# Kernel tuning notes

Measured on AMD Instinct MI355X. Metric: run time of the kernel, lower is better.

The kernel has to match this reference:

```python
import jax, jax.numpy as jnp
import numpy as np

B, N, H, DK, DV = 2, 2048, 16, 128, 128
E = H * DV
EPS = 1e-6


def setup_inputs() -> dict:
    key = jax.random.key(0)
    ks = jax.random.split(key, 8)
    sc_qk = 1.0 / np.sqrt(E + H * DK)  # xavier_normal-ish std
    sc_e = 1.0 / np.sqrt(2 * E)
    d = {
        "x": jax.random.normal(ks[0], (B, N, E), jnp.float32),
        "Wq": jax.random.normal(ks[1], (H * DK, E), jnp.float32) * sc_qk,
        "bq": jnp.zeros((H * DK,), jnp.float32),
        "Wk": jax.random.normal(ks[2], (H * DK, E), jnp.float32) * sc_qk,
        "bk": jnp.zeros((H * DK,), jnp.float32),
        "Wv": jax.random.normal(ks[3], (E, E), jnp.float32) * sc_e,
        "bv": jnp.zeros((E,), jnp.float32),
        "Wg": jax.random.normal(ks[4], (E, E), jnp.float32) * sc_e,
        "bg": jnp.zeros((E,), jnp.float32),
        "Wo": jax.random.normal(ks[5], (E, E), jnp.float32) * sc_e,
        "bo": jnp.zeros((E,), jnp.float32),
        "start_idx": 0,
    }
    return d


def _retention_scan(q, k, v, decays):
    # q,k: [B,N,H,DK] (k already scaled), v: [B,N,H,DV]
    qs = jnp.moveaxis(q, 1, 0)  # [N,B,H,DK]
    ks_ = jnp.moveaxis(k, 1, 0)
    vs = jnp.moveaxis(v, 1, 0)
    dec = decays[None, :, None, None]  # [1,H,1,1]

    def step(state, qkv):
        qt, kt, vt = qkv
        # state_n = decay * state_{n-1} + k_n (x) v_n
        state = dec * state + kt[..., :, None] * vt[..., None, :]  # [B,H,DK,DV]
        ret = jnp.einsum("bhk,bhkv->bhv", qt, state)
        return state, ret

    init = jnp.zeros((q.shape[0], H, DK, DV), q.dtype)
    final_state, rets = jax.lax.scan(step, init, (qs, ks_, vs))
    return jnp.moveaxis(rets, 0, 1), final_state  # [B,N,H,DV], [B,H,DK,DV]


def reference(x, Wq, bq, Wk, bk, Wv, bv, Wg, bg, Wo, bo, start_idx):
    b, n, _ = x.shape
    decays = 1.0 - jnp.exp2(-5.0 - jnp.arange(H, dtype=jnp.float32))  # [H]
    q = (x @ Wq.T + bq).reshape(b, n, H, DK)
    k = (x @ Wk.T + bk).reshape(b, n, H, DK) / (DK ** 0.5)
    v = (x @ Wv.T + bv).reshape(b, n, H, DV)
    retention, state = _retention_scan(q, k, v, decays)
    # GroupNorm over (b n) tokens, num_groups=H, channels=E, no affine
    r = retention.reshape(b * n, H, DV).astype(jnp.float32)
    mu = jnp.mean(r, axis=-1, keepdims=True)
    var = jnp.var(r, axis=-1, keepdims=True)
    r = (r - mu) / jnp.sqrt(var + EPS)
    r = r.reshape(b, n, E).astype(x.dtype)
    gate = jax.nn.silu(x @ Wg.T + bg)
    out = (r * gate) @ Wo.T + bo
    return out, state
```

## Files before the change

kernel.cpp:

```cpp
#include <hip/hip_runtime.h>
#include <hip/hip_bf16.h>

typedef __attribute__((ext_vector_type(8))) short short8;
typedef __attribute__((ext_vector_type(4))) short short4v;
typedef __attribute__((ext_vector_type(4))) float floatx4;

#define DI __device__ __forceinline__

constexpr int B_ = 2, N_ = 2048, H_ = 16, DK_ = 128, DV_ = 128, E_ = 2048;
constexpr int M_ = B_ * N_;
constexpr int NCAT_ = 4 * E_;
constexpr int CH_ = 128;
constexpr int NC_ = N_ / CH_;
constexpr float KSCALE = 0.08838834764831845f;

constexpr long OFF_XB   = 0;
constexpr long OFF_WCAT = 16777216;
constexpr long OFF_WOB  = 50331648;
constexpr long OFF_BCAT = 58720256;
constexpr long OFF_Y    = 58753024;
constexpr long OFF_KT   = 125861888;
constexpr long OFF_VT   = 142639104;
constexpr long OFF_SCB  = 159416320;

DI unsigned short f2bf(float f){
  unsigned u = __float_as_uint(f);
  u += 0x7fffu + ((u >> 16) & 1u);
  return (unsigned short)(u >> 16);
}
DI float bf2f(unsigned short s){ return __uint_as_float(((unsigned)s) << 16); }

DI void gload_lds16(const void* g, void* l){
  __builtin_amdgcn_global_load_lds(
      (const __attribute__((address_space(1))) unsigned int*)g,
      (__attribute__((address_space(3))) unsigned int*)l, 16, 0, 0);
}

__global__ void k_castall(const float* __restrict__ x,
                          const float* __restrict__ Wq, const float* __restrict__ Wk,
                          const float* __restrict__ Wv, const float* __restrict__ Wg,
                          const float* __restrict__ Wo,
                          const float* __restrict__ bq, const float* __restrict__ bk,
                          const float* __restrict__ bv, const float* __restrict__ bg,
                          unsigned short* __restrict__ xb, unsigned short* __restrict__ Wcat,
                          unsigned short* __restrict__ Wob, float* __restrict__ bcat){
  int bid = blockIdx.x;
  if(bid >= 14336){
    int i = (bid - 14336) * 2048 + threadIdx.x * 8;
    #pragma unroll
    for(int u=0;u<8;++u){
      int j = i + u;
      float v;
      if(j < 2048)      v = bq[j];
      else if(j < 4096) v = bk[j - 2048];
      else if(j < 6144) v = bv[j - 4096];
      else              v = bg[j - 6144];
      bcat[j] = v;
    }
    return;
  }
  const float* s; unsigned short* d; long off;
  if(bid < 4096){ s = x; d = xb; off = (long)bid*2048; }
  else if(bid < 6144){ s = Wq; d = Wcat;            off = (long)(bid-4096)*2048; }
  else if(bid < 8192){ s = Wk; d = Wcat + 4194304L; off = (long)(bid-6144)*2048; }
  else if(bid < 10240){ s = Wv; d = Wcat + 8388608L; off = (long)(bid-8192)*2048; }
  else if(bid < 12288){ s = Wg; d = Wcat + 12582912L; off = (long)(bid-10240)*2048; }
  else { s = Wo; d = Wob; off = (long)(bid-12288)*2048; }
  long i = off + (long)threadIdx.x * 8;
  float4 v0 = *(const float4*)(s + i);
  float4 v1 = *(const float4*)(s + i + 4);
  short8 o;
  o[0]=(short)f2bf(v0.x); o[1]=(short)f2bf(v0.y); o[2]=(short)f2bf(v0.z); o[3]=(short)f2bf(v0.w);
  o[4]=(short)f2bf(v1.x); o[5]=(short)f2bf(v1.y); o[6]=(short)f2bf(v1.z); o[7]=(short)f2bf(v1.w);
  *(short8*)(d + i) = o;
}

__global__ __launch_bounds__(512, 2)
void k_gemm256(const unsigned short* __restrict__ A,
               const unsigned short* __restrict__ Bt,
               unsigned short* __restrict__ Y,
               const float* __restrict__ bias)
{
  extern __shared__ unsigned short lds[];
  constexpr int K = 2048;
  constexpr int NKT = K / 64;

  const int tid = threadIdx.x;
  const int wave = tid >> 6, lane = tid & 63;
  const int wr = wave >> 2, wc = wave & 3;
  const int l15 = lane & 15;

  int bid = blockIdx.x;
  int g = bid & 7, w = bid >> 3;
  int bm = (g & 1) * 8 + (w & 7);
  int bn = (g >> 1) * 8 + (w >> 3);

  const unsigned short* Ag = A  + (long)bm * 256 * K;
  const unsigned short* Bg = Bt + (long)bn * 256 * K;

  const int sr = (lane >> 3);
  const int sc = ((lane & 7) ^ sr) * 8;
  const int colx[2] = { ((0 + (lane>>4)) ^ (lane&7)) << 4,
                        ((4 + (lane>>4)) ^ (lane&7)) << 4 };

  floatx4 acc[8][4] = {};
  const char* ldsc = (const char*)lds;
  short8 Aa[8], Ab[8], Ba[4], Bb[4];

#define STG_A(buf, kt, mh) do{                                                        \
    _Pragma("unroll")                                                                 \
    for(int g2=0; g2<2; ++g2){                                                        \
      gload_lds16(Ag + (long)(wr*128 + (mh)*64 + wc*16 + g2*8 + sr)*K                 \
                     + (long)(kt)*64 + sc,                                            \
                  &lds[(buf)*16384 + wr*8192 + ((mh)*64 + wc*16 + g2*8)*64 + lane*8]);\
    }                                                                                 \
  }while(0)

#define STG_B(buf, kt, nh) do{                                                        \
    _Pragma("unroll")                                                                 \
    for(int g2=0; g2<2; ++g2){                                                        \
      gload_lds16(Bg + (long)(wc*64 + (nh)*32 + wr*16 + g2*8 + sr)*K                  \
                     + (long)(kt)*64 + sc,                                            \
                  &lds[32768 + (buf)*16384 + (wc>>1)*8192                             \
                       + ((wc&1)*64 + (nh)*32 + wr*16 + g2*8)*64 + lane*8]);          \
    }                                                                                 \
  }while(0)

#define RD_A(dst, buf, mh) do{                                                        \
    const char* _b = ldsc + ((buf)*16384 + wr*8192)*2;                                \
    _Pragma("unroll")                                                                 \
    for(int ai=0; ai<4; ++ai){                                                        \
      const int _rb = ((mh)*64 + ai*16 + l15) << 7;                                   \
      dst[ai*2+0] = *(const short8*)(_b + _rb + colx[0]);                             \
      dst[ai*2+1] = *(const short8*)(_b + _rb + colx[1]);                             \
    }                                                                                 \
  }while(0)

#define RD_B(dst, buf, nh) do{                                                        \
    const char* _b = ldsc + (32768 + (buf)*16384 + (wc>>1)*8192)*2;                   \
    _Pragma("unroll")                                                                 \
    for(int bj=0; bj<2; ++bj){                                                        \
      const int _rb = ((wc&1)*64 + (nh)*32 + bj*16 + l15) << 7;                       \
      dst[bj*2+0] = *(const short8*)(_b + _rb + colx[0]);                             \
      dst[bj*2+1] = *(const short8*)(_b + _rb + colx[1]);                             \
    }                                                                                 \
  }while(0)

#define MFQ(mh, nh, As, Bs) do{                                                       \
    __builtin_amdgcn_s_setprio(1);                                                    \
    _Pragma("unroll")                                                                 \
    for(int ai=0; ai<4; ++ai)                                                         \
      _Pragma("unroll")                                                               \
      for(int bj=0; bj<2; ++bj)                                                       \
        _Pragma("unroll")                                                             \
        for(int kk=0; kk<2; ++kk)                                                     \
          acc[(mh)*4+ai][(nh)*2+bj] = __builtin_amdgcn_mfma_f32_16x16x32_bf16(        \
              As[ai*2+kk], Bs[bj*2+kk], acc[(mh)*4+ai][(nh)*2+bj], 0,0,0);            \
    __builtin_amdgcn_s_setprio(0);                                                    \
  }while(0)

#define VM4   asm volatile("s_waitcnt vmcnt(4)" ::: "memory")
#define BAR   __builtin_amdgcn_s_barrier()
#define SCHED __builtin_amdgcn_sched_barrier(0)

  STG_A(0, 0, 0); STG_B(0, 0, 0); STG_B(0, 0, 1); STG_A(0, 0, 1);
  VM4;
  BAR;
  SCHED;

  #pragma unroll 1
  for(int i=0; i<NKT/2; ++i){
    const int t1 = 2*i + 1;
    const int t2 = (2*i + 2) & (NKT - 1);

    RD_A(Aa, 0, 0); RD_B(Ba, 0, 0);
    STG_A(1, t1, 0); STG_B(1, t1, 0);
    VM4; BAR;
    MFQ(0, 0, Aa, Ba);
    BAR; SCHED;
    RD_B(Bb, 0, 1);
    STG_B(1, t1, 1);
    VM4; BAR;
    MFQ(0, 1, Aa, Bb);
    BAR; SCHED;
    RD_A(Ab, 0, 1);
    STG_A(1, t1, 1);
    VM4; BAR;
    MFQ(1, 1, Ab, Bb);
    BAR; SCHED;
    VM4; BAR;
    MFQ(1, 0, Ab, Ba);
    BAR; SCHED;

    RD_A(Aa, 1, 0); RD_B(Ba, 1, 0);
    STG_A(0, t2, 0); STG_B(0, t2, 0);
    VM4; BAR;
    MFQ(0, 0, Aa, Ba);
    BAR; SCHED;
    RD_B(Bb, 1, 1);
    STG_B(0, t2, 1);
    VM4; BAR;
    MFQ(0, 1, Aa, Bb);
    BAR; SCHED;
    RD_A(Ab, 1, 1);
    STG_A(0, t2, 1);
    VM4; BAR;
    MFQ(1, 1, Ab, Bb);
    BAR; SCHED;
    VM4; BAR;
    MFQ(1, 0, Ab, Ba);
    BAR; SCHED;
  }
#undef STG_A
#undef STG_B
#undef RD_A
#undef RD_B
#undef MFQ
#undef VM4
#undef BAR
#undef SCHED

  #pragma unroll
  for(int mh=0;mh<2;++mh){
    #pragma unroll
    for(int ai=0;ai<4;++ai){
      const int rowi = bm*256 + wr*128 + mh*64 + ai*16 + ((lane>>4)<<2);
      #pragma unroll
      for(int nh=0;nh<2;++nh){
        #pragma unroll
        for(int bj=0;bj<2;++bj){
          const int col = bn*256 + wc*64 + nh*32 + bj*16 + l15;
          const float bs = bias[col];
          const int sec = col >> 11;
          #pragma unroll
          for(int r=0;r<4;++r){
            float v = acc[mh*4+ai][nh*2+bj][r] + bs;
            if(sec == 1) v *= KSCALE;
            else if(sec == 3) v = v / (1.f + __expf(-v));
            Y[(long)(rowi + r) * NCAT_ + col] = f2bf(v);
          }
        }
      }
    }
  }
}

template<int EPI>
__global__ __launch_bounds__(256)
void k_gemm(const unsigned short* __restrict__ A,
            const unsigned short* __restrict__ Bt,
            void* __restrict__ outp,
            const float* __restrict__ bias,
            int M, int Ncols, int K, int NB)
{
  __shared__ unsigned short lA[2*128*64];
  __shared__ unsigned short lB[2*128*64];
  const int bid = blockIdx.x;
  const int bm = bid / NB, bn = bid % NB;
  const int tid = threadIdx.x;
  const int wave = tid >> 6, lane = tid & 63;
  const int wr = wave >> 1, wc = wave & 1;

  floatx4 acc[4][4] = {};

  int srow[4], scol[4];
  #pragma unroll
  for(int is=0; is<4; ++is){
    int o = is*4096 + wave*1024 + lane*16;
    int row = o >> 7;
    int logcb = (o & 127) ^ ((row & 7) << 4);
    srow[is] = row; scol[is] = logcb >> 1;
  }
  const unsigned short* Abase = A + (long)bm * 128 * K;
  const unsigned short* Bbase = Bt + (long)bn * 128 * K;

#define STG128(kt, buf) do{                                                          \
    const int _k0 = (kt) << 6;                                                       \
    _Pragma("unroll")                                                                \
    for(int is=0; is<4; ++is){                                                       \
      gload_lds16(Abase + (long)srow[is]*K + _k0 + scol[is], &lA[(buf)*8192 + ((is*4096 + wave*1024) >> 1)]); \
      gload_lds16(Bbase + (long)srow[is]*K + _k0 + scol[is], &lB[(buf)*8192 + ((is*4096 + wave*1024) >> 1)]); \
    }                                                                                \
  }while(0)

  const int nkt = K >> 6;
  STG128(0, 0);
  for(int kt=0; kt<nkt; ++kt){
    const int cur = kt & 1, nxt = cur ^ 1;
    const int ktn = (kt + 1 == nkt) ? 0 : kt + 1;
    __syncthreads();
    STG128(ktn, nxt);
    const char* cA = (const char*)lA + cur*16384;
    const char* cB = (const char*)lB + cur*16384;
    #pragma unroll
    for(int kk=0; kk<2; ++kk){
      const int cb = (kk<<6) + ((lane>>4)<<4);
      short8 af[4], bfr[4];
      #pragma unroll
      for(int i=0;i<4;++i){
        int row = (wr<<6) + (i<<4) + (lane&15);
        af[i] = *(const short8*)(cA + (row<<7) + (cb ^ ((row&7)<<4)));
      }
      #pragma unroll
      for(int j=0;j<4;++j){
        int row = (wc<<6) + (j<<4) + (lane&15);
        bfr[j] = *(const short8*)(cB + (row<<7) + (cb ^ ((row&7)<<4)));
      }
      #pragma unroll
      for(int i=0;i<4;++i)
        #pragma unroll
        for(int j=0;j<4;++j)
          acc[i][j] = __builtin_amdgcn_mfma_f32_16x16x32_bf16(af[i], bfr[j], acc[i][j], 0,0,0);
    }
  }
#undef STG128

  #pragma unroll
  for(int i=0;i<4;++i){
    #pragma unroll
    for(int j=0;j<4;++j){
      #pragma unroll
      for(int r=0;r<4;++r){
        int row = bm*128 + (wr<<6) + (i<<4) + ((lane>>4)<<2) + r;
        int col = bn*128 + (wc<<6) + (j<<4) + (lane&15);
        float v = acc[i][j][r] + bias[col];
        if(EPI == 0){
          int sec = col >> 11;
          if(sec == 1) v *= KSCALE;
          else if(sec == 3) v = v / (1.f + __expf(-v));
          ((unsigned short*)outp)[(long)row * Ncols + col] = f2bf(v);
        } else {
          ((float*)outp)[(long)row * Ncols + col] = v;
        }
      }
    }
  }
}

__global__ __launch_bounds__(256)
void k_chunksumT(const unsigned short* __restrict__ Y,
                 unsigned short* __restrict__ Vt,
                 float* __restrict__ MS){
  __shared__ unsigned short lt[64][136];
  __shared__ unsigned short Kt2[128][72];
  __shared__ unsigned short Vt2[128][72];
  int bid = blockIdx.x;
  int bh = bid >> 4, c = bid & 15, b = bh >> 4, h = bh & 15;
  int tid = threadIdx.x, wave = tid >> 6, lane = tid & 63;
  int wr = wave >> 1, wc = wave & 1;
  float dec = 1.f - exp2f(-5.f - (float)h);
  float l2d = log2f(dec);

  floatx4 acc[4][4] = {};

  #pragma unroll 1
  for(int h2 = 0; h2 < 2; ++h2){
    #pragma unroll
    for(int p=0;p<4;++p){
      int tl = p*16 + (tid>>4);
      int t  = h2*64 + tl;
      long row = ((long)(b*N_ + c*CH_ + t))*NCAT_ + 2048 + h*128 + (tid&15)*8;
      short8 v = *(const short8*)(Y + row);
      float f = exp2f(-(float)t * l2d);
      #pragma unroll
      for(int u=0;u<8;++u) v[u] = (short)f2bf(bf2f((unsigned short)v[u]) * f);
      *(short8*)&lt[tl][(tid&15)*8] = v;
    }
    __syncthreads();
    #pragma unroll
    for(int p=0;p<4;++p){
      int dk = p*32 + (tid>>3);
      int tc = (tid&7)*8;
      short8 o;
      #pragma unroll
      for(int u=0;u<8;++u) o[u] = (short)lt[tc+u][dk];
      *(short8*)&Kt2[dk][tc] = o;
    }
    __syncthreads();
    #pragma unroll
    for(int p=0;p<4;++p){
      int tl = p*16 + (tid>>4);
      int t  = h2*64 + tl;
      long row = ((long)(b*N_ + c*CH_ + t))*NCAT_ + 4096 + h*128 + (tid&15)*8;
      *(short8*)&lt[tl][(tid&15)*8] = *(const short8*)(Y + row);
    }
    __syncthreads();
    #pragma unroll
    for(int p=0;p<4;++p){
      int dv = p*32 + (tid>>3);
      int tc = (tid&7)*8;
      short8 o;
      #pragma unroll
      for(int u=0;u<8;++u) o[u] = (short)lt[tc+u][dv];
      *(short8*)&Vt2[dv][tc] = o;
      *(short8*)(Vt + ((long)(bh*128 + dv))*N_ + c*CH_ + h2*64 + tc) = o;
    }
    __syncthreads();
    #pragma unroll
    for(int kk=0;kk<2;++kk){
      int tl = kk*32 + ((lane>>4)<<3);
      short8 af[4], bfr[4];
      #pragma unroll
      for(int i=0;i<4;++i){ int dv = (wr<<6)+(i<<4)+(lane&15); af[i]  = *(const short8*)&Vt2[dv][tl]; }
      #pragma unroll
      for(int j=0;j<4;++j){ int dk = (wc<<6)+(j<<4)+(lane&15); bfr[j] = *(const short8*)&Kt2[dk][tl]; }
      #pragma unroll
      for(int i=0;i<4;++i)
        #pragma unroll
        for(int j=0;j<4;++j)
          acc[i][j] = __builtin_amdgcn_mfma_f32_16x16x32_bf16(af[i], bfr[j], acc[i][j], 0,0,0);
    }
    __syncthreads();
  }

  float scale = exp2f(127.f * log2f(dec));
  float* Mo = MS + ((long)bh*NC_ + c) * 16384;
  #pragma unroll
  for(int i=0;i<4;++i)
    #pragma unroll
    for(int j=0;j<4;++j)
      #pragma unroll
      for(int r=0;r<4;++r){
        int dv = (wr<<6)+(i<<4)+((lane>>4)<<2)+r;
        int dk = (wc<<6)+(j<<4)+(lane&15);
        Mo[dv*128 + dk] = acc[i][j][r] * scale;
      }
}

__global__ __launch_bounds__(256)
void k_scan(const float* __restrict__ MS, unsigned short* __restrict__ Scb,
            float* __restrict__ stateOut){
  int bid = blockIdx.x;
  int bh = bid >> 4, p = bid & 15;
  int tid = threadIdx.x, h = bh & 15;
  float dec = 1.f - exp2f(-5.f - (float)h);
  float decC = exp2f(128.f * log2f(dec));
  int e0 = p*1024 + tid*4;
  floatx4 S = {0.f, 0.f, 0.f, 0.f};
  const float* base = MS + (long)bh * NC_ * 16384 + e0;
  unsigned short* sb = Scb + (long)bh * NC_ * 16384 + e0;
  for(int c=0;c<NC_;++c){
    floatx4 m = *(const floatx4*)(base + (long)c*16384);
    short4v q;
    #pragma unroll
    for(int u=0;u<4;++u) q[u] = (short)f2bf(S[u]);
    *(short4v*)(sb + (long)c*16384) = q;
    S = decC * S + m;
  }
  int dv = e0 >> 7, dk = e0 & 127;
  float* so = stateOut + (long)bh*16384 + dv;
  #pragma unroll
  for(int u=0;u<4;++u) so[(long)(dk+u)*128] = S[u];
}

__global__ __launch_bounds__(256)
void k_ret(const unsigned short* __restrict__ Y, const unsigned short* __restrict__ Vt,
           const unsigned short* __restrict__ Scb, unsigned short* __restrict__ RG){
  __shared__ unsigned short sQ[128*128];
  __shared__ unsigned short sK[128*128];
  int bid = blockIdx.x;
  int bh = bid >> 4, c = bid & 15, b = bh >> 4, h = bh & 15;
  int tid = threadIdx.x, w = tid >> 6, lane = tid & 63;
  float dec = 1.f - exp2f(-5.f - (float)h);
  float l2d = log2f(dec);

  #pragma unroll
  for(int p=0;p<8;++p){
    int t = p*16 + (tid>>4);
    long row = (long)(b*N_ + c*CH_ + t) * NCAT_ + h*128 + (tid&15)*8;
    short8 qv = *(const short8*)(Y + row);
    short8 kv = *(const short8*)(Y + row + 2048);
    float fq = exp2f((float)t * l2d);
    float fk = exp2f(-(float)t * l2d);
    short8 qs, ks;
    #pragma unroll
    for(int u=0;u<8;++u){
      qs[u] = (short)f2bf(bf2f((unsigned short)qv[u]) * fq);
      ks[u] = (short)f2bf(bf2f((unsigned short)kv[u]) * fk);
    }
    int ad = t*256 + (((tid&15)*16) ^ ((t&7)<<4));
    *(short8*)((char*)sQ + ad) = qs;
    *(short8*)((char*)sK + ad) = ks;
  }
  __syncthreads();

  floatx4 acc[2][8] = {};
  #pragma unroll
  for(int kk=0;kk<4;++kk){
    int cb = (kk<<6) + ((lane>>4)<<4);
    short8 af[2], bfr[8];
    #pragma unroll
    for(int i=0;i<2;++i){ int t = w*32 + (i<<4) + (lane&15); af[i] = *(const short8*)((const char*)sQ + t*256 + (cb ^ ((t&7)<<4))); }
    #pragma unroll
    for(int j=0;j<8;++j){ int s = (j<<4) + (lane&15); bfr[j] = *(const short8*)((const char*)sK + s*256 + (cb ^ ((s&7)<<4))); }
    #pragma unroll
    for(int i=0;i<2;++i)
      #pragma unroll
      for(int j=0;j<8;++j)
        acc[i][j] = __builtin_amdgcn_mfma_f32_16x16x32_bf16(af[i], bfr[j], acc[i][j], 0,0,0);
  }
  __syncthreads();

  #pragma unroll
  for(int i=0;i<2;++i)
    #pragma unroll
    for(int j=0;j<8;++j)
      #pragma unroll
      for(int r=0;r<4;++r){
        int t = w*32 + (i<<4) + ((lane>>4)<<2) + r;
        int s = (j<<4) + (lane&15);
        float v = (s <= t) ? acc[i][j][r] : 0.f;
        *(unsigned short*)((char*)sK + t*256 + ((s*2) ^ ((t&7)<<4))) = f2bf(v);
      }
  __syncthreads();

  #pragma unroll
  for(int i=0;i<2;++i)
    #pragma unroll
    for(int j=0;j<8;++j)
      #pragma unroll
      for(int u=0;u<4;++u) acc[i][j][u] = 0.f;

  const unsigned short* Vb = Vt + (long)bh*128*N_ + c*CH_;
  #pragma unroll
  for(int kk=0;kk<4;++kk){
    int cb = (kk<<6) + ((lane>>4)<<4);
    int sg = kk*32 + ((lane>>4)<<3);
    short8 af[2], bfr[8];
    #pragma unroll
    for(int i=0;i<2;++i){ int t = w*32 + (i<<4) + (lane&15); af[i] = *(const short8*)((const char*)sK + t*256 + (cb ^ ((t&7)<<4))); }
    #pragma unroll
    for(int j=0;j<8;++j){ int dv = (j<<4) + (lane&15); bfr[j] = *(const short8*)(Vb + (long)dv*N_ + sg); }
    #pragma unroll
    for(int i=0;i<2;++i)
      #pragma unroll
      for(int j=0;j<8;++j)
        acc[i][j] = __builtin_amdgcn_mfma_f32_16x16x32_bf16(af[i], bfr[j], acc[i][j], 0,0,0);
  }
  const unsigned short* Sb = Scb + ((long)bh*NC_ + c) * 16384;
  #pragma unroll
  for(int kk=0;kk<4;++kk){
    int cb = (kk<<6) + ((lane>>4)<<4);
    int kg = kk*32 + ((lane>>4)<<3);
    short8 af[2], bfr[8];
    #pragma unroll
    for(int i=0;i<2;++i){
      int t = w*32 + (i<<4) + (lane&15);
      short8 qv = *(const short8*)((const char*)sQ + t*256 + (cb ^ ((t&7)<<4)));
      #pragma unroll
      for(int u=0;u<8;++u) af[i][u] = (short)f2bf(bf2f((unsigned short)qv[u]) * dec);
    }
    #pragma unroll
    for(int j=0;j<8;++j){ int dv = (j<<4) + (lane&15); bfr[j] = *(const short8*)(Sb + (long)dv*128 + kg); }
    #pragma unroll
    for(int i=0;i<2;++i)
      #pragma unroll
      for(int j=0;j<8;++j)
        acc[i][j] = __builtin_amdgcn_mfma_f32_16x16x32_bf16(af[i], bfr[j], acc[i][j], 0,0,0);
  }

  #pragma unroll
  for(int i=0;i<2;++i){
    #pragma unroll
    for(int r=0;r<4;++r){
      float s1 = 0.f, s2 = 0.f;
      #pragma unroll
      for(int j=0;j<8;++j){ float v = acc[i][j][r]; s1 += v; s2 += v*v; }
      #pragma unroll
      for(int off=1; off<16; off<<=1){ s1 += __shfl_xor(s1, off); s2 += __shfl_xor(s2, off); }
      float mu  = s1 * (1.f/128.f);
      float var = s2 * (1.f/128.f) - mu*mu;
      float inv = rsqrtf(var + 1e-6f);
      int t = w*32 + (i<<4) + ((lane>>4)<<2) + r;
      long mrow = (long)(b*N_ + c*CH_ + t);
      #pragma unroll
      for(int j=0;j<8;++j){
        int dv = (j<<4) + (lane&15);
        float v = (acc[i][j][r] - mu) * inv;
        float g = bf2f(Y[mrow*NCAT_ + 6144 + h*128 + dv]);
        RG[mrow*E_ + h*128 + dv] = f2bf(v * g);
      }
    }
  }
}

extern "C" void kernel_launch(void* const* d_in, const int* in_sizes, int n_in,
                              void* d_out, int out_size, void* d_ws, size_t ws_size,
                              hipStream_t stream) {
  const float* x  = (const float*)d_in[0];
  const float* Wq = (const float*)d_in[1];
  const float* bq = (const float*)d_in[2];
  const float* Wk = (const float*)d_in[3];
  const float* bk = (const float*)d_in[4];
  const float* Wv = (const float*)d_in[5];
  const float* bv = (const float*)d_in[6];
  const float* Wg = (const float*)d_in[7];
  const float* bg = (const float*)d_in[8];
  const float* Wo = (const float*)d_in[9];
  const float* bo = (const float*)d_in[10];

  char* ws = (char*)d_ws;
  unsigned short* xb   = (unsigned short*)(ws + OFF_XB);
  unsigned short* Wcat = (unsigned short*)(ws + OFF_WCAT);
  unsigned short* Wob  = (unsigned short*)(ws + OFF_WOB);
  float*          bcat = (float*)(ws + OFF_BCAT);
  unsigned short* Y    = (unsigned short*)(ws + OFF_Y);
  unsigned short* Vt   = (unsigned short*)(ws + OFF_VT);
  unsigned short* Scb  = (unsigned short*)(ws + OFF_SCB);
  float*          MS   = (float*)(ws + OFF_WCAT);
  unsigned short* RG   = (unsigned short*)(ws + OFF_XB);

  float* outp     = (float*)d_out;
  float* stateOut = outp + (long)M_ * E_;

  (void)hipFuncSetAttribute((const void*)k_gemm256,
                            hipFuncAttributeMaxDynamicSharedMemorySize, 131072);

  k_castall<<<14340, 256, 0, stream>>>(x, Wq, Wk, Wv, Wg, Wo, bq, bk, bv, bg,
                                       xb, Wcat, Wob, bcat);

  k_gemm256<<<512, 512, 131072, stream>>>(xb, Wcat, Y, bcat);

  k_chunksumT<<<512, 256, 0, stream>>>(Y, Vt, MS);

  k_scan<<<512, 256, 0, stream>>>(MS, Scb, stateOut);

  k_ret<<<512, 256, 0, stream>>>(Y, Vt, Scb, RG);

  k_gemm<1><<<(M_/128)*(E_/128), 256, 0, stream>>>(RG, Wob, (void*)outp, bo, M_, E_, E_, E_/128);
}
```

Baseline: 261.3 us.

## Replace output GEMM with 256x128 pipelined kernel and store chunk states in bf16

The generic 128x128 output projection GEMM is replaced by a 512-thread kernel with 256x128 tiles, swizzled LDS staging, explicit vmcnt waits and barriers, split B-fragment reads interleaved with MFMA, and a grouped block ordering for L2 reuse. Separately, the per-chunk state matrices written by chunksumT and read by scan are stored as bf16 instead of fp32, halving that intermediate traffic. The bf16 chunk states add rounding error to the carried recurrent state, and the hand-scheduled GEMM depends on exact wait counts for correctness.

```diff
diff --git a/kernel.cpp b/kernel.cpp
--- a/kernel.cpp
+++ b/kernel.cpp
@@ -19,7 +19,6 @@
 constexpr long OFF_WOB  = 50331648;
 constexpr long OFF_BCAT = 58720256;
 constexpr long OFF_Y    = 58753024;
-constexpr long OFF_KT   = 125861888;
 constexpr long OFF_VT   = 142639104;
 constexpr long OFF_SCB  = 159416320;
 
@@ -245,94 +244,128 @@
   }
 }
 
-template<int EPI>
-__global__ __launch_bounds__(256)
-void k_gemm(const unsigned short* __restrict__ A,
-            const unsigned short* __restrict__ Bt,
-            void* __restrict__ outp,
-            const float* __restrict__ bias,
-            int M, int Ncols, int K, int NB)
+__global__ __launch_bounds__(512, 2)
+void k_gemm2(const unsigned short* __restrict__ A,
+             const unsigned short* __restrict__ Bt,
+             float* __restrict__ outp,
+             const float* __restrict__ bias)
 {
-  __shared__ unsigned short lA[2*128*64];
-  __shared__ unsigned short lB[2*128*64];
-  const int bid = blockIdx.x;
-  const int bm = bid / NB, bn = bid % NB;
+  extern __shared__ unsigned short lds[];
+  constexpr int K = 2048;
+  constexpr int NKT = K / 64;
+
   const int tid = threadIdx.x;
   const int wave = tid >> 6, lane = tid & 63;
-  const int wr = wave >> 1, wc = wave & 1;
+  const int wm = wave >> 1, wn = wave & 1;
+  const int l15 = lane & 15;
+
+  int bid = blockIdx.x;
+  int g = bid & 7, w = bid >> 3;
+  int bm = (g & 1) * 8 + (w & 7);
+  int bn = (g >> 1) * 4 + (w >> 3);
+
+  const unsigned short* Ag = A  + (long)bm * 256 * K;
+  const unsigned short* Bg = Bt + (long)bn * 128 * K;
+
+  const int sr = lane >> 3;
+  const int sc = ((lane & 7) ^ sr) * 8;
+  const int colx[2] = { (((lane>>4)  ) ^ (lane&7)) << 4,
+                        (((lane>>4)+4) ^ (lane&7)) << 4 };
 
   floatx4 acc[4][4] = {};
-
-  int srow[4], scol[4];
-  #pragma unroll
-  for(int is=0; is<4; ++is){
-    int o = is*4096 + wave*1024 + lane*16;
-    int row = o >> 7;
-    int logcb = (o & 127) ^ ((row & 7) << 4);
-    srow[is] = row; scol[is] = logcb >> 1;
-  }
-  const unsigned short* Abase = A + (long)bm * 128 * K;
-  const unsigned short* Bbase = Bt + (long)bn * 128 * K;
-
-#define STG128(kt, buf) do{                                                          \
-    const int _k0 = (kt) << 6;                                                       \
-    _Pragma("unroll")                                                                \
-    for(int is=0; is<4; ++is){                                                       \
-      gload_lds16(Abase + (long)srow[is]*K + _k0 + scol[is], &lA[(buf)*8192 + ((is*4096 + wave*1024) >> 1)]); \
-      gload_lds16(Bbase + (long)srow[is]*K + _k0 + scol[is], &lB[(buf)*8192 + ((is*4096 + wave*1024) >> 1)]); \
-    }                                                                                \
-  }while(0)
-
-  const int nkt = K >> 6;
-  STG128(0, 0);
-  for(int kt=0; kt<nkt; ++kt){
-    const int cur = kt & 1, nxt = cur ^ 1;
-    const int ktn = (kt + 1 == nkt) ? 0 : kt + 1;
-    __syncthreads();
-    STG128(ktn, nxt);
-    const char* cA = (const char*)lA + cur*16384;
-    const char* cB = (const char*)lB + cur*16384;
-    #pragma unroll
-    for(int kk=0; kk<2; ++kk){
-      const int cb = (kk<<6) + ((lane>>4)<<4);
-      short8 af[4], bfr[4];
-      #pragma unroll
-      for(int i=0;i<4;++i){
-        int row = (wr<<6) + (i<<4) + (lane&15);
-        af[i] = *(const short8*)(cA + (row<<7) + (cb ^ ((row&7)<<4)));
-      }
-      #pragma unroll
-      for(int j=0;j<4;++j){
-        int row = (wc<<6) + (j<<4) + (lane&15);
-        bfr[j] = *(const short8*)(cB + (row<<7) + (cb ^ ((row&7)<<4)));
-      }
-      #pragma unroll
-      for(int i=0;i<4;++i)
-        #pragma unroll
-        for(int j=0;j<4;++j)
-          acc[i][j] = __builtin_amdgcn_mfma_f32_16x16x32_bf16(af[i], bfr[j], acc[i][j], 0,0,0);
-    }
-  }
-#undef STG128
-
-  #pragma unroll
-  for(int i=0;i<4;++i){
-    #pragma unroll
-    for(int j=0;j<4;++j){
-      #pragma unroll
-      for(int r=0;r<4;++r){
-        int row = bm*128 + (wr<<6) + (i<<4) + ((lane>>4)<<2) + r;
-        int col = bn*128 + (wc<<6) + (j<<4) + (lane&15);
-        float v = acc[i][j][r] + bias[col];
-        if(EPI == 0){
-          int sec = col >> 11;
-          if(sec == 1) v *= KSCALE;
-          else if(sec == 3) v = v / (1.f + __expf(-v));
-          ((unsigned short*)outp)[(long)row * Ncols + col] = f2bf(v);
-        } else {
-          ((float*)outp)[(long)row * Ncols + col] = v;
-        }
-      }
+  const char* ldsc = (const char*)lds;
+  short8 Av[8], Bv[4], Bw[4];
+
+#define STG_AB(buf, kt) do{                                                           \
+    _Pragma("unroll")                                                                 \
+    for(int g2=0; g2<4; ++g2){                                                        \
+      gload_lds16(Ag + (long)(wm*64 + wn*32 + g2*8 + sr)*K + (long)(kt)*64 + sc,      \
+                  &lds[(buf)*16384 + (wm*64 + wn*32 + g2*8)*64 + lane*8]);            \
+    }                                                                                 \
+    _Pragma("unroll")                                                                 \
+    for(int g2=0; g2<2; ++g2){                                                        \
+      gload_lds16(Bg + (long)(wn*64 + wm*16 + g2*8 + sr)*K + (long)(kt)*64 + sc,      \
+                  &lds[32768 + (buf)*8192 + (wn*64 + wm*16 + g2*8)*64 + lane*8]);     \
+    }                                                                                 \
+  }while(0)
+
+#define RD_A2(buf) do{                                                                \
+    const char* _b = ldsc + (buf)*32768;                                              \
+    _Pragma("unroll")                                                                 \
+    for(int ai=0; ai<4; ++ai){                                                        \
+      const int _rb = (wm*64 + ai*16 + l15) << 7;                                     \
+      Av[ai*2+0] = *(const short8*)(_b + _rb + colx[0]);                              \
+      Av[ai*2+1] = *(const short8*)(_b + _rb + colx[1]);                              \
+    }                                                                                 \
+  }while(0)
+
+#define RD_B2(dst, buf, half) do{                                                     \
+    const char* _b = ldsc + 65536 + (buf)*16384;                                      \
+    _Pragma("unroll")                                                                 \
+    for(int bj=0; bj<2; ++bj){                                                        \
+      const int _rb = (wn*64 + ((half)*2+bj)*16 + l15) << 7;                          \
+      dst[bj*2+0] = *(const short8*)(_b + _rb + colx[0]);                             \
+      dst[bj*2+1] = *(const short8*)(_b + _rb + colx[1]);                             \
+    }                                                                                 \
+  }while(0)
+
+#define MF8(half, Bs) do{                                                             \
+    __builtin_amdgcn_s_setprio(1);                                                    \
+    _Pragma("unroll")                                                                 \
+    for(int ai=0; ai<4; ++ai)                                                         \
+      _Pragma("unroll")                                                               \
+      for(int bj=0; bj<2; ++bj)                                                       \
+        _Pragma("unroll")                                                             \
+        for(int kk=0; kk<2; ++kk)                                                     \
+          acc[ai][(half)*2+bj] = __builtin_amdgcn_mfma_f32_16x16x32_bf16(             \
+              Av[ai*2+kk], Bs[bj*2+kk], acc[ai][(half)*2+bj], 0,0,0);                 \
+    __builtin_amdgcn_s_setprio(0);                                                    \
+  }while(0)
+
+#define VM6   asm volatile("s_waitcnt vmcnt(6)" ::: "memory")
+#define BAR   __builtin_amdgcn_s_barrier()
+#define SCHED __builtin_amdgcn_sched_barrier(0)
+
+  STG_AB(0, 0);
+
+  #pragma unroll 1
+  for(int i=0; i<NKT/2; ++i){
+    const int u = 2*i;
+    STG_AB(1, u+1);
+    VM6; BAR;
+    RD_A2(0); RD_B2(Bv, 0, 0);
+    MF8(0, Bv);
+    SCHED;
+    RD_B2(Bw, 0, 1);
+    MF8(1, Bw);
+    BAR; SCHED;
+    STG_AB(0, (u+2) & (NKT-1));
+    VM6; BAR;
+    RD_A2(1); RD_B2(Bv, 1, 0);
+    MF8(0, Bv);
+    SCHED;
+    RD_B2(Bw, 1, 1);
+    MF8(1, Bw);
+    BAR; SCHED;
+  }
+#undef STG_AB
+#undef RD_A2
+#undef RD_B2
+#undef MF8
+#undef VM6
+#undef BAR
+#undef SCHED
+
+  #pragma unroll
+  for(int ai=0;ai<4;++ai){
+    const int row = bm*256 + wm*64 + ai*16 + ((lane>>4)<<2);
+    #pragma unroll
+    for(int bj=0;bj<4;++bj){
+      const int col = bn*128 + wn*64 + bj*16 + l15;
+      const float bs = bias[col];
+      #pragma unroll
+      for(int r=0;r<4;++r)
+        outp[(long)(row + r)*E_ + col] = acc[ai][bj][r] + bs;
     }
   }
 }
@@ -340,7 +373,7 @@
 __global__ __launch_bounds__(256)
 void k_chunksumT(const unsigned short* __restrict__ Y,
                  unsigned short* __restrict__ Vt,
-                 float* __restrict__ MS){
+                 unsigned short* __restrict__ MS){
   __shared__ unsigned short lt[64][136];
   __shared__ unsigned short Kt2[128][72];
   __shared__ unsigned short Vt2[128][72];
@@ -414,7 +447,7 @@
   }
 
   float scale = exp2f(127.f * log2f(dec));
-  float* Mo = MS + ((long)bh*NC_ + c) * 16384;
+  unsigned short* Mo = MS + ((long)bh*NC_ + c) * 16384;
   #pragma unroll
   for(int i=0;i<4;++i)
     #pragma unroll
@@ -423,12 +456,12 @@
       for(int r=0;r<4;++r){
         int dv = (wr<<6)+(i<<4)+((lane>>4)<<2)+r;
         int dk = (wc<<6)+(j<<4)+(lane&15);
-        Mo[dv*128 + dk] = acc[i][j][r] * scale;
+        Mo[dv*128 + dk] = f2bf(acc[i][j][r] * scale);
       }
 }
 
 __global__ __launch_bounds__(256)
-void k_scan(const float* __restrict__ MS, unsigned short* __restrict__ Scb,
+void k_scan(const unsigned short* __restrict__ MS, unsigned short* __restrict__ Scb,
             float* __restrict__ stateOut){
   int bid = blockIdx.x;
   int bh = bid >> 4, p = bid & 15;
@@ -437,15 +470,16 @@
   float decC = exp2f(128.f * log2f(dec));
   int e0 = p*1024 + tid*4;
   floatx4 S = {0.f, 0.f, 0.f, 0.f};
-  const float* base = MS + (long)bh * NC_ * 16384 + e0;
+  const unsigned short* base = MS + (long)bh * NC_ * 16384 + e0;
   unsigned short* sb = Scb + (long)bh * NC_ * 16384 + e0;
   for(int c=0;c<NC_;++c){
-    floatx4 m = *(const floatx4*)(base + (long)c*16384);
+    short4v m = *(const short4v*)(base + (long)c*16384);
     short4v q;
     #pragma unroll
     for(int u=0;u<4;++u) q[u] = (short)f2bf(S[u]);
     *(short4v*)(sb + (long)c*16384) = q;
-    S = decC * S + m;
+    #pragma unroll
+    for(int u=0;u<4;++u) S[u] = decC * S[u] + bf2f((unsigned short)m[u]);
   }
   int dv = e0 >> 7, dk = e0 & 127;
   float* so = stateOut + (long)bh*16384 + dv;
@@ -607,7 +641,7 @@
   unsigned short* Y    = (unsigned short*)(ws + OFF_Y);
   unsigned short* Vt   = (unsigned short*)(ws + OFF_VT);
   unsigned short* Scb  = (unsigned short*)(ws + OFF_SCB);
-  float*          MS   = (float*)(ws + OFF_WCAT);
+  unsigned short* MS   = (unsigned short*)(ws + OFF_WCAT);
   unsigned short* RG   = (unsigned short*)(ws + OFF_XB);
 
   float* outp     = (float*)d_out;
@@ -615,6 +649,8 @@
 
   (void)hipFuncSetAttribute((const void*)k_gemm256,
                             hipFuncAttributeMaxDynamicSharedMemorySize, 131072);
+  (void)hipFuncSetAttribute((const void*)k_gemm2,
+                            hipFuncAttributeMaxDynamicSharedMemorySize, 98304);
 
   k_castall<<<14340, 256, 0, stream>>>(x, Wq, Wk, Wv, Wg, Wo, bq, bk, bv, bg,
                                        xb, Wcat, Wob, bcat);
@@ -627,5 +663,5 @@
 
   k_ret<<<512, 256, 0, stream>>>(Y, Vt, Scb, RG);
 
-  k_gemm<1><<<(M_/128)*(E_/128), 256, 0, stream>>>(RG, Wob, (void*)outp, bo, M_, E_, E_, E_/128);
-}
+  k_gemm2<<<256, 512, 98304, stream>>>(RG, Wob, outp, bo);
+}
```

After: 252.7 us. 3.3% less time.
